# Performance work log

Measured on AMD Instinct MI355X. Metric: run time of the kernel, lower is better.

## Reference

```python
import jax
import jax.numpy as jnp
import numpy as np
import math

KNN = 16
DIST_THRESH = 0.03


def setup_inputs() -> dict:
    key = jax.random.key(0)
    ks = jax.random.split(key, 7)
    B, N, M = 2, 8192, 8192
    Din, D = 64, 64
    feature1 = jax.random.normal(ks[0], (B, N, Din), dtype=jnp.float32)
    xyz1 = jax.random.uniform(ks[1], (B, N, 3), dtype=jnp.float32)
    xyz2 = jax.random.uniform(ks[2], (B, M, 3), dtype=jnp.float32)
    Wp = jax.random.normal(ks[3], (Din, D), dtype=jnp.float32) * 0.05
    bp = jnp.zeros((D,), dtype=jnp.float32)
    W1 = jax.random.normal(ks[4], (3, D), dtype=jnp.float32) * 0.05
    b1 = jnp.zeros((D,), dtype=jnp.float32)
    W2 = jax.random.normal(ks[5], (D, D), dtype=jnp.float32) * 0.05
    b2 = jnp.zeros((D,), dtype=jnp.float32)
    return {"feature1": feature1, "xyz1": xyz1, "xyz2": xyz2,
            "Wp": Wp, "bp": bp, "W1": W1, "b1": b1, "W2": W2, "b2": b2}


def reference(feature1, xyz1, xyz2, Wp, bp, W1, b1, W2, b2):
    # prefix linear: [B,N,Din] -> [B,N,D]
    f = feature1 @ Wp + bp

    # knn_point: squared pairwise distance from queries xyz2 to points xyz1
    # d2: [B, M, N]
    d2 = (jnp.sum(xyz2 * xyz2, axis=-1)[:, :, None]
          + jnp.sum(xyz1 * xyz1, axis=-1)[:, None, :]
          - 2.0 * jnp.einsum('bmd,bnd->bmn', xyz2, xyz1))
    neg_d, idx = jax.lax.top_k(-d2, KNN)        # smallest-k, ascending
    dist = -neg_d                                # [B, M, KNN]

    min_distance = dist[:, :, 0]                 # [B, M]
    weight = jnp.where(min_distance > DIST_THRESH, 10.0, 1.0).astype(f.dtype)

    # index_points: per-batch gather of neighbor features / coords
    g_feature = jax.vmap(lambda a, i: a[i])(f, idx)      # [B, M, KNN, D]
    g_xyz = jax.vmap(lambda a, i: a[i])(xyz1, idx)       # [B, M, KNN, 3]
    g_xyz = g_xyz - xyz2[:, :, None, :]                  # relative coords

    # fc_position MLP: 3 -> D -> D
    pw = jax.nn.relu(g_xyz @ W1 + b1) @ W2 + b2          # [B, M, KNN, D]

    # per-channel weighted reduction over KNN neighbors
    new_feature = jnp.einsum('bmkc,bmkc->bmc', pw, g_feature) / math.sqrt(KNN)
    return new_feature, weight
```

## Files before the change

### kernel.cpp

```cpp
#include <hip/hip_runtime.h>
#include <math.h>

#define B 2
#define N 8192
#define M 8192
#define D 64
#define KNN 16
#define BM (B * M)
#define GC 16
#define NC (GC * GC * GC)
#define NSC 64
#define WTMAX 192
#define CAP 20
#define TCAP 448

using frag_ab = __attribute__((ext_vector_type(8))) short;
using frag_cd = __attribute__((ext_vector_type(4))) float;

__device__ __forceinline__ short f2bf(float x) {
    unsigned u = __float_as_uint(x);
    u += 0x7fffu + ((u >> 16) & 1u);
    return (short)(u >> 16);
}

__device__ __forceinline__ float query_cutr(float qx, float qy, float qz) {
    int nc = ((qx < 0.16f) | (qx > 0.84f)) + ((qy < 0.16f) | (qy > 0.84f))
           + ((qz < 0.16f) | (qz > 0.84f));
    return nc == 0 ? 0.121f : nc == 1 ? 0.1525f : nc == 2 ? 0.1921f : 0.242f;
}

#define CHAIN_INS(VARR, IARR, DVAL, IVAL) do {                          \
    float _dd = (DVAL); int _ii = (IVAL);                               \
    _Pragma("unroll")                                                   \
    for (int _r = 0; _r < KNN; ++_r) {                                  \
        bool  _sm = _dd < VARR[_r];                                     \
        float _tv = VARR[_r]; int _ti = IARR[_r];                       \
        VARR[_r] = _sm ? _dd : _tv;  IARR[_r] = _sm ? _ii : _ti;        \
        _dd      = _sm ? _tv : _dd;  _ii      = _sm ? _ti : _ii;        \
    }                                                                   \
} while (0)
#define CHAIN_INSERT(DVAL, IVAL) CHAIN_INS(v, id, DVAL, IVAL)

#define BITONIC_ROUND(VARR, IARR, DL) do {                              \
    float _nv[KNN]; int _nid[KNN];                                      \
    _Pragma("unroll")                                                   \
    for (int _i = 0; _i < KNN; ++_i) {                                  \
        float _pv = __shfl_xor(VARR[KNN - 1 - _i], (DL), 64);           \
        int   _pi = __shfl_xor(IARR[KNN - 1 - _i], (DL), 64);           \
        bool _tk = VARR[_i] <= _pv;                                     \
        _nv[_i]  = _tk ? VARR[_i] : _pv;                                \
        _nid[_i] = _tk ? IARR[_i] : _pi;                                \
    }                                                                   \
    _Pragma("unroll")                                                   \
    for (int _st = 8; _st; _st >>= 1) {                                 \
        _Pragma("unroll")                                               \
        for (int _i = 0; _i < KNN; ++_i) {                              \
            if (!(_i & _st)) {                                          \
                int _j = _i | _st;                                      \
                bool _sw = _nv[_i] > _nv[_j];                           \
                float _ta = _sw ? _nv[_j] : _nv[_i];                    \
                float _tb = _sw ? _nv[_i] : _nv[_j];                    \
                int _ia = _sw ? _nid[_j] : _nid[_i];                    \
                int _ib = _sw ? _nid[_i] : _nid[_j];                    \
                _nv[_i] = _ta; _nv[_j] = _tb;                           \
                _nid[_i] = _ia; _nid[_j] = _ib;                         \
            }                                                           \
        }                                                               \
    }                                                                   \
    _Pragma("unroll")                                                   \
    for (int _i = 0; _i < KNN; ++_i) { VARR[_i] = _nv[_i]; IARR[_i] = _nid[_i]; } \
} while (0)

#define KPROC(PV, TV) do {                                              \
    float _dx = (PV).x - qx, _dy = (PV).y - qy, _dz = (PV).z - qz;      \
    float _dv = fmaf(_dx, _dx, fmaf(_dy, _dy, _dz * _dz));              \
    if (_dv < fcut) {                                                   \
        if (cnt < CAP) {                                                \
            ibuf[cnt][lane] = (unsigned short)(TV);                     \
            ++cnt;                                                      \
        } else {                                   \
            CHAIN_INSERT(_dv, __float_as_int((PV).w));                  \
        }                                                               \
    }                                                                   \
} while (0)

#define KFLUSH() do {                                                   \
    int _t = 0;                                                         \
    for (; _t + 4 <= cur; _t += 4) {                                    \
        float4 _q0 = tile[_t + 0], _q1 = tile[_t + 1];                  \
        float4 _q2 = tile[_t + 2], _q3 = tile[_t + 3];                  \
        KPROC(_q0, _t + 0); KPROC(_q1, _t + 1);                         \
        KPROC(_q2, _t + 2); KPROC(_q3, _t + 3);                         \
    }                                                                   \
    for (; _t < cur; ++_t) { float4 _q0 = tile[_t]; KPROC(_q0, _t); }   \
    int _mx = cnt;                                                      \
    _Pragma("unroll")                                                   \
    for (int _o = 32; _o; _o >>= 1)                                     \
        _mx = max(_mx, __shfl_xor(_mx, _o, 64));                        \
    _mx = __builtin_amdgcn_readfirstlane(_mx);                          \
    int _t2 = 0;                                                        \
    for (; _t2 + 2 <= _mx; _t2 += 2) {                                  \
        int _ta = (_t2     < cnt) ? (int)ibuf[_t2    ][lane] : 0;       \
        int _tb = (_t2 + 1 < cnt) ? (int)ibuf[_t2 + 1][lane] : 0;       \
        float4 _pa = tile[_ta], _pb = tile[_tb];   \
        float _dxa = _pa.x - qx, _dya = _pa.y - qy, _dza = _pa.z - qz;  \
        float _dva = fmaf(_dxa, _dxa, fmaf(_dya, _dya, _dza * _dza));   \
        if (_t2 < cnt && _dva < v[KNN - 1])                             \
            CHAIN_INSERT(_dva, __float_as_int(_pa.w));                  \
        float _dxb = _pb.x - qx, _dyb = _pb.y - qy, _dzb = _pb.z - qz;  \
        float _dvb = fmaf(_dxb, _dxb, fmaf(_dyb, _dyb, _dzb * _dzb));   \
        if (_t2 + 1 < cnt && _dvb < v[KNN - 1])                         \
            CHAIN_INSERT(_dvb, __float_as_int(_pb.w));                  \
    }                                                                   \
    for (; _t2 < _mx; ++_t2) {                                          \
        int _tp = (_t2 < cnt) ? (int)ibuf[_t2][lane] : 0;               \
        float4 _p = tile[_tp];                                          \
        float _dx = _p.x - qx, _dy = _p.y - qy, _dz = _p.z - qz;        \
        float _dv = fmaf(_dx, _dx, fmaf(_dy, _dy, _dz * _dz));          \
        if (_t2 < cnt && _dv < v[KNN - 1])                              \
            CHAIN_INSERT(_dv, __float_as_int(_p.w));                    \
    }                                                                   \
    cnt = 0; cur = 0;                                                   \
} while (0)

__global__ __launch_bounds__(256) void k_prep(const float* __restrict__ feat,
                                              const float* __restrict__ Wp,
                                              const float* __restrict__ bp,
                                              const float* __restrict__ xyz1,
                                              const float* __restrict__ xyz2,
                                              unsigned* __restrict__ pcount,
                                              unsigned* __restrict__ qcount,
                                              float* __restrict__ f) {
    if (blockIdx.x < 64) {
        int i = blockIdx.x * 256 + threadIdx.x;
        int b = i >> 13;
        const float* p = xyz1 + (size_t)i * 3;
        int cx = max(0, min(GC - 1, (int)(p[0] * GC)));
        int cy = max(0, min(GC - 1, (int)(p[1] * GC)));
        int cz = max(0, min(GC - 1, (int)(p[2] * GC)));
        atomicAdd(&pcount[b * NC + (cz * GC + cy) * GC + cx], 1u);
        const float* q = xyz2 + (size_t)i * 3;
        int qx = max(0, min(GC - 1, (int)(q[0] * GC)));
        int qy = max(0, min(GC - 1, (int)(q[1] * GC)));
        int qz = max(0, min(GC - 1, (int)(q[2] * GC)));
        int sc = ((qz >> 2) * 4 + (qy >> 2)) * 4 + (qx >> 2);
        atomicAdd(&qcount[b * NSC + sc], 1u);
    }
    int c  = threadIdx.x & 63;
    int wv = threadIdx.x >> 6;
    int row0 = blockIdx.x * 32 + wv * 8;
    float wp[64];
#pragma unroll
    for (int d = 0; d < 64; ++d) wp[d] = Wp[d * 64 + c];
    float bpc = bp[c];
    float fv[8], acc[8];
#pragma unroll
    for (int r = 0; r < 8; ++r) {
        fv[r]  = feat[(size_t)(row0 + r) * 64 + c];
        acc[r] = bpc;
    }
#pragma unroll
    for (int d = 0; d < 64; ++d) {
#pragma unroll
        for (int r = 0; r < 8; ++r)
            acc[r] = fmaf(__shfl(fv[r], d, 64), wp[d], acc[r]);
    }
#pragma unroll
    for (int r = 0; r < 8; ++r)
        f[(size_t)(row0 + r) * 64 + c] = acc[r];
}

__global__ __launch_bounds__(256) void k_scan(const unsigned* __restrict__ pcount,
                                              const unsigned* __restrict__ qcount,
                                              unsigned* __restrict__ pstart,
                                              unsigned* __restrict__ pcur,
                                              unsigned* __restrict__ qcur,
                                              int* __restrict__ wtab,
                                              int* __restrict__ ntab) {
    __shared__ unsigned wsum[4];
    int blk = blockIdx.x;
    if (blk < 2) {
        int b = blk;
        int t = threadIdx.x;
        int base = b * NC + t * 16;
        unsigned c[16]; unsigned tsum = 0;
#pragma unroll
        for (int k = 0; k < 16; ++k) { c[k] = pcount[base + k]; tsum += c[k]; }
        int lane = t & 63, wv = t >> 6;
        unsigned x = tsum;
#pragma unroll
        for (int off = 1; off < 64; off <<= 1) {
            unsigned y = __shfl_up(x, off, 64);
            if (lane >= off) x += y;
        }
        if (lane == 63) wsum[wv] = x;
        __syncthreads();
        unsigned pre = 0;
        for (int k2 = 0; k2 < wv; ++k2) pre += wsum[k2];
        unsigned run = pre + x - tsum;
#pragma unroll
        for (int k = 0; k < 16; ++k) {
            pstart[base + k] = run; pcur[base + k] = run; run += c[k];
        }
    } else {
        int b = blk - 2;
        if (threadIdx.x >= 64) return;
        int lane = threadIdx.x;
        int c = (int)qcount[b * NSC + lane];
        int x = c;
#pragma unroll
        for (int off = 1; off < 64; off <<= 1) {
            int y = __shfl_up(x, off, 64);
            if (lane >= off) x += y;
        }
        int run = x - c;
        qcur[b * NSC + lane] = (unsigned)run;
        int ne = (c + 63) >> 6;
        int e = ne;
#pragma unroll
        for (int off = 1; off < 64; off <<= 1) {
            int y = __shfl_up(e, off, 64);
            if (lane >= off) e += y;
        }
        int eoff = e - ne;
        for (int j = 0; j < ne; ++j)
            wtab[b * WTMAX + eoff + j] = ((run + j * 64) << 7) | min(64, c - j * 64);
        if (lane == 63) ntab[b] = eoff + ne;
    }
}

__global__ __launch_bounds__(256) void k_scatter(const float* __restrict__ xyz1,
                                                 const float* __restrict__ xyz2,
                                                 unsigned* __restrict__ pcur,
                                                 unsigned* __restrict__ qcur,
                                                 float4* __restrict__ spts,
                                                 int* __restrict__ sidx,
                                                 float4* __restrict__ squery) {
    int i = blockIdx.x * 256 + threadIdx.x;
    int b = i >> 13;
    const float* p = xyz1 + (size_t)i * 3;
    float x = p[0], y = p[1], z = p[2];
    int cx = max(0, min(GC - 1, (int)(x * GC)));
    int cy = max(0, min(GC - 1, (int)(y * GC)));
    int cz = max(0, min(GC - 1, (int)(z * GC)));
    unsigned pos = atomicAdd(&pcur[b * NC + (cz * GC + cy) * GC + cx], 1u);
    spts[(size_t)b * N + pos] = make_float4(x, y, z, fmaf(x, x, fmaf(y, y, z * z)));
    sidx[(size_t)b * N + pos] = i & (N - 1);

    const float* q = xyz2 + (size_t)i * 3;
    float qx = q[0], qy = q[1], qz = q[2];
    int ax = max(0, min(GC - 1, (int)(qx * GC)));
    int ay = max(0, min(GC - 1, (int)(qy * GC)));
    int az = max(0, min(GC - 1, (int)(qz * GC)));
    int sc = ((az >> 2) * 4 + (ay >> 2)) * 4 + (ax >> 2);
    unsigned qpos = atomicAdd(&qcur[b * NSC + sc], 1u);
    squery[(size_t)b * M + qpos] = make_float4(qx, qy, qz, __int_as_float(i));
}

template <int NSLT>
__global__ __launch_bounds__(64) void k_knn(const float4* __restrict__ spts,
                                            const float4* __restrict__ squery,
                                            const unsigned* __restrict__ pstart,
                                            const unsigned* __restrict__ pcount,
                                            const int* __restrict__ wtab,
                                            const int* __restrict__ ntab,
                                            float* __restrict__ part_d,
                                            int* __restrict__ part_i) {
    __shared__ float4         tile[TCAP];
    __shared__ unsigned short ibuf[CAP][64];
    int bid = blockIdx.x;
    int b   = bid / (WTMAX * NSLT);
    int rem = bid - b * (WTMAX * NSLT);
    int ti  = rem / NSLT;
    int s   = rem % NSLT;
    if (ti >= ntab[b]) return;
    int e = wtab[b * WTMAX + ti];
    int qnum = e & 127, qoff = (e >> 7) & 0x3FFF;
    int lane = threadIdx.x;

    int sl = lane < qnum ? lane : qnum - 1;
    float4 q4 = squery[(size_t)b * M + qoff + sl];
    float qx = q4.x, qy = q4.y, qz = q4.z;
    float cutr = query_cutr(qx, qy, qz);
    float fcut = cutr * cutr;

    int lx0 = max(0, (int)floorf((qx - cutr) * GC));
    int lx1 = min(GC - 1, (int)floorf((qx + cutr) * GC));
    int ly0 = max(0, (int)floorf((qy - cutr) * GC));
    int ly1 = min(GC - 1, (int)floorf((qy + cutr) * GC));
    int lz0 = max(0, (int)floorf((qz - cutr) * GC));
    int lz1 = min(GC - 1, (int)floorf((qz + cutr) * GC));
#pragma unroll
    for (int off = 1; off < 64; off <<= 1) {
        lx0 = min(lx0, __shfl_xor(lx0, off, 64));
        lx1 = max(lx1, __shfl_xor(lx1, off, 64));
        ly0 = min(ly0, __shfl_xor(ly0, off, 64));
        ly1 = max(ly1, __shfl_xor(ly1, off, 64));
        lz0 = min(lz0, __shfl_xor(lz0, off, 64));
        lz1 = max(lz1, __shfl_xor(lz1, off, 64));
    }
    int bx0 = __builtin_amdgcn_readfirstlane(lx0);
    int bx1 = __builtin_amdgcn_readfirstlane(lx1);
    int by0 = __builtin_amdgcn_readfirstlane(ly0);
    int by1 = __builtin_amdgcn_readfirstlane(ly1);
    int bz0 = __builtin_amdgcn_readfirstlane(lz0);
    int bz1 = __builtin_amdgcn_readfirstlane(lz1);

    float v[KNN]; int id[KNN];
#pragma unroll
    for (int r = 0; r < KNN; ++r) { v[r] = 3.4e38f; id[r] = 0; }
    int cnt = 0, cur = 0;
    int pb = b * N, cb = b * NC;
    int xspan = bx1 - bx0;

    int ny = by1 - by0 + 1;
    int nrows = (bz1 - bz0 + 1) * ny;
    int myrows = (s < nrows) ? ((nrows - 1 - s) / NSLT + 1) : 0;
    int stj = 0, enj = 0;
    {
        int rj = s + NSLT * lane;
        if (lane < myrows) {
            int dz = rj / ny;
            int dy = rj - dz * ny;
            int codeL = cb + ((bz0 + dz) * GC + (by0 + dy)) * GC + bx0;
            stj = (int)pstart[codeL];
            enj = (int)pstart[codeL + xspan] + (int)pcount[codeL + xspan];
        }
    }
    for (int j = 0; j < myrows; ++j) {
        int st = __builtin_amdgcn_readfirstlane(__shfl(stj, j, 64));
        int en = __builtin_amdgcn_readfirstlane(__shfl(enj, j, 64));
        int len = en - st;
        if (cur + len > TCAP) KFLUSH();
        for (int u = lane; u < len; u += 64) {
            float4 p = spts[pb + st + u];
            p.w = __int_as_float(st + u);
            tile[cur + u] = p;
        }
        cur += len;
    }
    KFLUSH();

    if (lane < qnum) {
        size_t base = ((size_t)(b * M + qoff + lane) * NSLT + s) * KNN;
        float4* pd = (float4*)(part_d + base);
        int4*   pi = (int4*)(part_i + base);
#pragma unroll
        for (int r4 = 0; r4 < 4; ++r4) {
            pd[r4] = make_float4(v[r4 * 4 + 0], v[r4 * 4 + 1],
                                 v[r4 * 4 + 2], v[r4 * 4 + 3]);
            pi[r4] = make_int4(id[r4 * 4 + 0], id[r4 * 4 + 1],
                               id[r4 * 4 + 2], id[r4 * 4 + 3]);
        }
    }
}

template <int NSLT>
__global__ __launch_bounds__(256, 4) void k_merge(const float4* __restrict__ squery,
                                                  const float* __restrict__ part_d,
                                                  const int* __restrict__ part_i,
                                                  const int* __restrict__ sidx,
                                                  const float4* __restrict__ spts,
                                                  int* __restrict__ idx_out,
                                                  float* __restrict__ w_out) {
    int tid = threadIdx.x;
    int l   = tid & 63;
    int wv  = tid >> 6;
    int g   = l >> 4;
    int gl  = l & 15;
    int sqid = blockIdx.x * 16 + wv * 4 + g;
    int b = sqid >> 13;

    float v[KNN]; int id[KNN];
    if (gl < NSLT) {
        size_t base = ((size_t)sqid * NSLT + gl) * KNN;
        const float4* pd = (const float4*)(part_d + base);
        const int4*   pi = (const int4*)(part_i + base);
#pragma unroll
        for (int r4 = 0; r4 < 4; ++r4) {
            float4 dv = pd[r4]; int4 iv = pi[r4];
            v[r4 * 4 + 0] = dv.x; v[r4 * 4 + 1] = dv.y;
            v[r4 * 4 + 2] = dv.z; v[r4 * 4 + 3] = dv.w;
            id[r4 * 4 + 0] = iv.x; id[r4 * 4 + 1] = iv.y;
            id[r4 * 4 + 2] = iv.z; id[r4 * 4 + 3] = iv.w;
        }
    } else {
#pragma unroll
        for (int r = 0; r < KNN; ++r) { v[r] = 3.4e38f; id[r] = 0; }
    }
    BITONIC_ROUND(v, id, 1);
    BITONIC_ROUND(v, id, 2);
    BITONIC_ROUND(v, id, 4);
    BITONIC_ROUND(v, id, 8);

    float4 q4 = squery[sqid];
    float cutr = query_cutr(q4.x, q4.y, q4.z);
    bool miss = !(v[KNN - 1] < cutr * cutr * 0.9999f);
    int gq = __float_as_int(q4.w);
    if (!miss) {
        if (gl == 0) w_out[gq] = (v[0] > 0.03f) ? 10.0f : 1.0f;
        int myid = 0;
#pragma unroll
        for (int r = 0; r < KNN; ++r) if (gl == r) myid = id[r];
        idx_out[(size_t)gl * BM + sqid] = sidx[b * N + myid];
    }

    unsigned long long mmask = __ballot(miss && gl == 0);
    while (mmask) {
        int ml = __ffsll(mmask) - 1;
        mmask &= mmask - 1;
        int msq = blockIdx.x * 16 + wv * 4 + (ml >> 4);
        int mb = msq >> 13;
        float4 mq = squery[msq];
        float fv2[KNN]; int fi2[KNN];
#pragma unroll
        for (int r = 0; r < KNN; ++r) { fv2[r] = 3.4e38f; fi2[r] = 0; }
        for (int t = l; t < N; t += 64) {
            float4 p = spts[(size_t)mb * N + t];
            float dx = p.x - mq.x, dy = p.y - mq.y, dz = p.z - mq.z;
            float dv = fmaf(dx, dx, fmaf(dy, dy, dz * dz));
            if (dv < fv2[KNN - 1]) CHAIN_INS(fv2, fi2, dv, t);
        }
        BITONIC_ROUND(fv2, fi2, 1);
        BITONIC_ROUND(fv2, fi2, 2);
        BITONIC_ROUND(fv2, fi2, 4);
        BITONIC_ROUND(fv2, fi2, 8);
        BITONIC_ROUND(fv2, fi2, 16);
        BITONIC_ROUND(fv2, fi2, 32);
        int mgq = __float_as_int(mq.w);
        if (l == 0) w_out[mgq] = (fv2[0] > 0.03f) ? 10.0f : 1.0f;
        if (l < 16) {
            int myid = 0;
#pragma unroll
            for (int r = 0; r < KNN; ++r) if (l == r) myid = fi2[r];
            idx_out[(size_t)l * BM + msq] = sidx[mb * N + myid];
        }
    }
}

__global__ __launch_bounds__(256) void k_final(const float4* __restrict__ squery,
                                               const int* __restrict__ idxs,
                                               const float* __restrict__ xyz1,
                                               const float* __restrict__ f,
                                               const float* __restrict__ W1,
                                               const float* __restrict__ b1,
                                               const float* __restrict__ W2,
                                               const float* __restrict__ b2,
                                               float* __restrict__ out) {
    __shared__ __align__(16) unsigned short hT[4][16][72];
    int tid = threadIdx.x;
    int l   = tid & 63;
    int wv  = tid >> 6;
    int ln  = l & 15, lg = l >> 4;
    int mq  = blockIdx.x * 4 + wv;
    int bb  = mq >> 13;
    float4 q4 = squery[mq];
    int gq = __float_as_int(q4.w);
    float qx = q4.x, qy = q4.y, qz = q4.z;

    frag_ab bfrag[4][2];
#pragma unroll
    for (int t = 0; t < 4; ++t)
#pragma unroll
        for (int s = 0; s < 2; ++s) {
            frag_ab bv;
#pragma unroll
            for (int j = 0; j < 8; ++j)
                bv[j] = f2bf(W2[(lg * 8 + j + 32 * s) * 64 + t * 16 + ln]);
            bfrag[t][s] = bv;
        }

    float w10 = W1[l], w11 = W1[64 + l], w12 = W1[128 + l], b1c = b1[l];

#pragma unroll
    for (int k = 0; k < KNN; ++k) {
        int nk = idxs[(size_t)k * BM + mq];
        const float* p = xyz1 + ((size_t)bb * N + nk) * 3;
        float gx = p[0] - qx, gy = p[1] - qy, gz = p[2] - qz;
        float t = fmaf(gx, w10, b1c);
        t = fmaf(gy, w11, t);
        t = fmaf(gz, w12, t);
        hT[wv][k][l] = (unsigned short)f2bf(fmaxf(t, 0.f));
    }

    frag_cd acc[4];
#pragma unroll
    for (int t = 0; t < 4; ++t) acc[t] = (frag_cd){0.f, 0.f, 0.f, 0.f};
#pragma unroll
    for (int s = 0; s < 2; ++s) {
        frag_ab af = *(const frag_ab*)&hT[wv][ln][lg * 8 + 32 * s];
#pragma unroll
        for (int t = 0; t < 4; ++t)
            acc[t] = __builtin_amdgcn_mfma_f32_16x16x32_bf16(af, bfrag[t][s],
                                                             acc[t], 0, 0, 0);
    }

    int nk4[4];
#pragma unroll
    for (int i = 0; i < 4; ++i)
        nk4[i] = idxs[(size_t)(lg * 4 + i) * BM + mq];

#pragma unroll
    for (int t = 0; t < 4; ++t) {
        float b2c = b2[t * 16 + ln];
        float s = 0.f;
#pragma unroll
        for (int i = 0; i < 4; ++i) {
            float gf = f[((size_t)bb * N + nk4[i]) * 64 + t * 16 + ln];
            s = fmaf(acc[t][i] + b2c, gf, s);
        }
        s += __shfl_xor(s, 16, 64);
        s += __shfl_xor(s, 32, 64);
        if (lg == t)
            out[(size_t)gq * 64 + t * 16 + ln] = s * 0.25f;
    }
}

extern "C" void kernel_launch(void* const* d_in, const int* in_sizes, int n_in,
                              void* d_out, int out_size, void* d_ws, size_t ws_size,
                              hipStream_t stream) {
    const float* feature1 = (const float*)d_in[0];
    const float* xyz1     = (const float*)d_in[1];
    const float* xyz2     = (const float*)d_in[2];
    const float* Wp       = (const float*)d_in[3];
    const float* bp       = (const float*)d_in[4];
    const float* W1       = (const float*)d_in[5];
    const float* b1       = (const float*)d_in[6];
    const float* W2       = (const float*)d_in[7];
    const float* b2       = (const float*)d_in[8];
    float* out = (float*)d_out;

    char* w = (char*)d_ws;
    float4*   spts   = (float4*)w;    w += (size_t)B * N * 16;
    float4*   squery = (float4*)w;    w += (size_t)B * M * 16;
    float*    f      = (float*)w;     w += (size_t)B * N * D * 4;
    int*      sidx   = (int*)w;       w += (size_t)B * N * 4;
    unsigned* pcount = (unsigned*)w;  w += (size_t)B * NC * 4;
    unsigned* qcount = (unsigned*)w;  w += (size_t)B * NSC * 4;
    unsigned* pstart = (unsigned*)w;  w += (size_t)B * NC * 4;
    unsigned* pcur   = (unsigned*)w;  w += (size_t)B * NC * 4;
    unsigned* qcur   = (unsigned*)w;  w += (size_t)B * NSC * 4;
    int*      wtab   = (int*)w;       w += (size_t)B * WTMAX * 4;
    int*      ntab   = (int*)w;       w += 16;

    size_t used_fixed = (size_t)(w - (char*)d_ws);
    size_t per_slice  = (size_t)KNN * BM * 8;
    size_t idxf_bytes = (size_t)KNN * BM * 4;
    int nsl = (ws_size >= used_fixed + 16 * per_slice + idxf_bytes) ? 16 : 8;

    float*    partd  = (float*)w;     w += (size_t)nsl * KNN * BM * 4;
    int*      parti  = (int*)w;       w += (size_t)nsl * KNN * BM * 4;
    int*      idxf   = (int*)w;       w += idxf_bytes;
    float*    w_out  = out + (size_t)BM * D;

    hipMemsetAsync(pcount, 0, (size_t)(B * NC + B * NSC) * 4, stream);

    k_prep<<<B * N / 32, 256, 0, stream>>>(feature1, Wp, bp, xyz1, xyz2,
                                           pcount, qcount, f);
    k_scan<<<4, 256, 0, stream>>>(pcount, qcount, pstart, pcur, qcur, wtab, ntab);
    k_scatter<<<BM / 256, 256, 0, stream>>>(xyz1, xyz2, pcur, qcur, spts, sidx, squery);
    if (nsl == 16) {
        k_knn<16><<<B * WTMAX * 16, 64, 0, stream>>>(spts, squery, pstart, pcount,
                                                     wtab, ntab, partd, parti);
        k_merge<16><<<BM / 16, 256, 0, stream>>>(squery, partd, parti, sidx, spts,
                                                 idxf, w_out);
    } else {
        k_knn<8><<<B * WTMAX * 8, 64, 0, stream>>>(spts, squery, pstart, pcount,
                                                   wtab, ntab, partd, parti);
        k_merge<8><<<BM / 16, 256, 0, stream>>>(squery, partd, parti, sidx, spts,
                                                idxf, w_out);
    }
    k_final<<<BM / 4, 256, 0, stream>>>(squery, idxf, xyz1, f,
                                        W1, b1, W2, b2, out);
}
```

Baseline: 197.5 us.

## Pack two KNN slice waves per block and raise slice count to 32

The KNN kernel now runs two 64-lane waves per 128-thread block, each handling a different spatial slice with its own shared tile. The tile and candidate buffer capacities are halved, and tile filling is chunked so a cell range can be split across flushes. When the workspace is large enough, the search is split into 32 slices, and the merge kernel is generalized to a variable group size. The aim is finer-grained parallelism and better occupancy in the neighbor search, at the cost of more partial results to write and merge and more frequent flushes.

```diff
diff --git a/kernel.cpp b/kernel.cpp
--- a/kernel.cpp
+++ b/kernel.cpp
@@ -11,8 +11,8 @@
 #define NC (GC * GC * GC)
 #define NSC 64
 #define WTMAX 192
-#define CAP 20
-#define TCAP 448
+#define CAP 12
+#define TCAP 224
 
 using frag_ab = __attribute__((ext_vector_type(8))) short;
 using frag_cd = __attribute__((ext_vector_type(4))) float;
@@ -76,7 +76,7 @@
     float _dv = fmaf(_dx, _dx, fmaf(_dy, _dy, _dz * _dz));              \
     if (_dv < fcut) {                                                   \
         if (cnt < CAP) {                                                \
-            ibuf[cnt][lane] = (unsigned short)(TV);                     \
+            ibuf[cnt][tidx] = (unsigned short)(TV);                     \
             ++cnt;                                                      \
         } else {                                   \
             CHAIN_INSERT(_dv, __float_as_int((PV).w));                  \
@@ -87,12 +87,12 @@
 #define KFLUSH() do {                                                   \
     int _t = 0;                                                         \
     for (; _t + 4 <= cur; _t += 4) {                                    \
-        float4 _q0 = tile[_t + 0], _q1 = tile[_t + 1];                  \
-        float4 _q2 = tile[_t + 2], _q3 = tile[_t + 3];                  \
+        float4 _q0 = tilew[_t + 0], _q1 = tilew[_t + 1];                \
+        float4 _q2 = tilew[_t + 2], _q3 = tilew[_t + 3];                \
         KPROC(_q0, _t + 0); KPROC(_q1, _t + 1);                         \
         KPROC(_q2, _t + 2); KPROC(_q3, _t + 3);                         \
     }                                                                   \
-    for (; _t < cur; ++_t) { float4 _q0 = tile[_t]; KPROC(_q0, _t); }   \
+    for (; _t < cur; ++_t) { float4 _q0 = tilew[_t]; KPROC(_q0, _t); }  \
     int _mx = cnt;                                                      \
     _Pragma("unroll")                                                   \
     for (int _o = 32; _o; _o >>= 1)                                     \
@@ -100,9 +100,9 @@
     _mx = __builtin_amdgcn_readfirstlane(_mx);                          \
     int _t2 = 0;                                                        \
     for (; _t2 + 2 <= _mx; _t2 += 2) {                                  \
-        int _ta = (_t2     < cnt) ? (int)ibuf[_t2    ][lane] : 0;       \
-        int _tb = (_t2 + 1 < cnt) ? (int)ibuf[_t2 + 1][lane] : 0;       \
-        float4 _pa = tile[_ta], _pb = tile[_tb];   \
+        int _ta = (_t2     < cnt) ? (int)ibuf[_t2    ][tidx] : 0;       \
+        int _tb = (_t2 + 1 < cnt) ? (int)ibuf[_t2 + 1][tidx] : 0;       \
+        float4 _pa = tilew[_ta], _pb = tilew[_tb]; \
         float _dxa = _pa.x - qx, _dya = _pa.y - qy, _dza = _pa.z - qz;  \
         float _dva = fmaf(_dxa, _dxa, fmaf(_dya, _dya, _dza * _dza));   \
         if (_t2 < cnt && _dva < v[KNN - 1])                             \
@@ -113,8 +113,8 @@
             CHAIN_INSERT(_dvb, __float_as_int(_pb.w));                  \
     }                                                                   \
     for (; _t2 < _mx; ++_t2) {                                          \
-        int _tp = (_t2 < cnt) ? (int)ibuf[_t2][lane] : 0;               \
-        float4 _p = tile[_tp];                                          \
+        int _tp = (_t2 < cnt) ? (int)ibuf[_t2][tidx] : 0;               \
+        float4 _p = tilew[_tp];                                         \
         float _dx = _p.x - qx, _dy = _p.y - qy, _dz = _p.z - qz;        \
         float _dv = fmaf(_dx, _dx, fmaf(_dy, _dy, _dz * _dz));          \
         if (_t2 < cnt && _dv < v[KNN - 1])                              \
@@ -258,25 +258,30 @@
 }
 
 template <int NSLT>
-__global__ __launch_bounds__(64) void k_knn(const float4* __restrict__ spts,
-                                            const float4* __restrict__ squery,
-                                            const unsigned* __restrict__ pstart,
-                                            const unsigned* __restrict__ pcount,
-                                            const int* __restrict__ wtab,
-                                            const int* __restrict__ ntab,
-                                            float* __restrict__ part_d,
-                                            int* __restrict__ part_i) {
-    __shared__ float4         tile[TCAP];
-    __shared__ unsigned short ibuf[CAP][64];
+__global__ __launch_bounds__(128) void k_knn(const float4* __restrict__ spts,
+                                             const float4* __restrict__ squery,
+                                             const unsigned* __restrict__ pstart,
+                                             const unsigned* __restrict__ pcount,
+                                             const int* __restrict__ wtab,
+                                             const int* __restrict__ ntab,
+                                             float* __restrict__ part_d,
+                                             int* __restrict__ part_i) {
+    __shared__ float4         tile2[2][TCAP];
+    __shared__ unsigned short ibuf[CAP][128];
+    constexpr int SPB = NSLT / 2;
+    int tidx = threadIdx.x;
+    int lane = tidx & 63;
+    int wv   = tidx >> 6;
     int bid = blockIdx.x;
-    int b   = bid / (WTMAX * NSLT);
-    int rem = bid - b * (WTMAX * NSLT);
-    int ti  = rem / NSLT;
-    int s   = rem % NSLT;
+    int b   = bid / (WTMAX * SPB);
+    int rem = bid - b * (WTMAX * SPB);
+    int ti  = rem / SPB;
+    int sp  = rem - ti * SPB;
+    int s   = sp * 2 + wv;
     if (ti >= ntab[b]) return;
+    float4* tilew = tile2[wv];
     int e = wtab[b * WTMAX + ti];
     int qnum = e & 127, qoff = (e >> 7) & 0x3FFF;
-    int lane = threadIdx.x;
 
     int sl = lane < qnum ? lane : qnum - 1;
     float4 q4 = squery[(size_t)b * M + qoff + sl];
@@ -331,13 +336,16 @@
         int st = __builtin_amdgcn_readfirstlane(__shfl(stj, j, 64));
         int en = __builtin_amdgcn_readfirstlane(__shfl(enj, j, 64));
         int len = en - st;
-        if (cur + len > TCAP) KFLUSH();
-        for (int u = lane; u < len; u += 64) {
-            float4 p = spts[pb + st + u];
-            p.w = __int_as_float(st + u);
-            tile[cur + u] = p;
-        }
-        cur += len;
+        while (len > 0) {
+            int take = min(len, TCAP - cur);
+            for (int u = lane; u < take; u += 64) {
+                float4 p = spts[pb + st + u];
+                p.w = __int_as_float(st + u);
+                tilew[cur + u] = p;
+            }
+            cur += take; st += take; len -= take;
+            if (cur == TCAP) KFLUSH();
+        }
     }
     KFLUSH();
 
@@ -363,17 +371,19 @@
                                                   const float4* __restrict__ spts,
                                                   int* __restrict__ idx_out,
                                                   float* __restrict__ w_out) {
+    constexpr int GS  = NSLT;
+    constexpr int QPW = 64 / GS;
     int tid = threadIdx.x;
     int l   = tid & 63;
     int wv  = tid >> 6;
-    int g   = l >> 4;
-    int gl  = l & 15;
-    int sqid = blockIdx.x * 16 + wv * 4 + g;
+    int g   = l / GS;
+    int gl  = l % GS;
+    int sqid = blockIdx.x * (QPW * 4) + wv * QPW + g;
     int b = sqid >> 13;
 
     float v[KNN]; int id[KNN];
-    if (gl < NSLT) {
-        size_t base = ((size_t)sqid * NSLT + gl) * KNN;
+    {
+        size_t base = ((size_t)sqid * GS + gl) * KNN;
         const float4* pd = (const float4*)(part_d + base);
         const int4*   pi = (const int4*)(part_i + base);
 #pragma unroll
@@ -384,14 +394,10 @@
             id[r4 * 4 + 0] = iv.x; id[r4 * 4 + 1] = iv.y;
             id[r4 * 4 + 2] = iv.z; id[r4 * 4 + 3] = iv.w;
         }
-    } else {
-#pragma unroll
-        for (int r = 0; r < KNN; ++r) { v[r] = 3.4e38f; id[r] = 0; }
-    }
-    BITONIC_ROUND(v, id, 1);
-    BITONIC_ROUND(v, id, 2);
-    BITONIC_ROUND(v, id, 4);
-    BITONIC_ROUND(v, id, 8);
+    }
+#pragma unroll
+    for (int dl = 1; dl < GS; dl <<= 1)
+        BITONIC_ROUND(v, id, dl);
 
     float4 q4 = squery[sqid];
     float cutr = query_cutr(q4.x, q4.y, q4.z);
@@ -399,17 +405,23 @@
     int gq = __float_as_int(q4.w);
     if (!miss) {
         if (gl == 0) w_out[gq] = (v[0] > 0.03f) ? 10.0f : 1.0f;
-        int myid = 0;
-#pragma unroll
-        for (int r = 0; r < KNN; ++r) if (gl == r) myid = id[r];
-        idx_out[(size_t)gl * BM + sqid] = sidx[b * N + myid];
+#pragma unroll
+        for (int rr = 0; rr < (KNN + GS - 1) / GS; ++rr) {
+            int r = gl + rr * GS;
+            if (r < KNN) {
+                int myid = 0;
+#pragma unroll
+                for (int k = 0; k < KNN; ++k) if (r == k) myid = id[k];
+                idx_out[(size_t)r * BM + sqid] = sidx[b * N + myid];
+            }
+        }
     }
 
     unsigned long long mmask = __ballot(miss && gl == 0);
     while (mmask) {
         int ml = __ffsll(mmask) - 1;
         mmask &= mmask - 1;
-        int msq = blockIdx.x * 16 + wv * 4 + (ml >> 4);
+        int msq = blockIdx.x * (QPW * 4) + wv * QPW + ml / GS;
         int mb = msq >> 13;
         float4 mq = squery[msq];
         float fv2[KNN]; int fi2[KNN];
@@ -546,7 +558,8 @@
     size_t used_fixed = (size_t)(w - (char*)d_ws);
     size_t per_slice  = (size_t)KNN * BM * 8;
     size_t idxf_bytes = (size_t)KNN * BM * 4;
-    int nsl = (ws_size >= used_fixed + 16 * per_slice + idxf_bytes) ? 16 : 8;
+    int nsl = (ws_size >= used_fixed + 32 * per_slice + idxf_bytes) ? 32 :
+              (ws_size >= used_fixed + 16 * per_slice + idxf_bytes) ? 16 : 8;
 
     float*    partd  = (float*)w;     w += (size_t)nsl * KNN * BM * 4;
     int*      parti  = (int*)w;       w += (size_t)nsl * KNN * BM * 4;
@@ -559,15 +572,20 @@
                                            pcount, qcount, f);
     k_scan<<<4, 256, 0, stream>>>(pcount, qcount, pstart, pcur, qcur, wtab, ntab);
     k_scatter<<<BM / 256, 256, 0, stream>>>(xyz1, xyz2, pcur, qcur, spts, sidx, squery);
-    if (nsl == 16) {
-        k_knn<16><<<B * WTMAX * 16, 64, 0, stream>>>(spts, squery, pstart, pcount,
+    if (nsl == 32) {
+        k_knn<32><<<B * WTMAX * 16, 128, 0, stream>>>(spts, squery, pstart, pcount,
+                                                      wtab, ntab, partd, parti);
+        k_merge<32><<<BM / 8, 256, 0, stream>>>(squery, partd, parti, sidx, spts,
+                                                idxf, w_out);
+    } else if (nsl == 16) {
+        k_knn<16><<<B * WTMAX * 8, 128, 0, stream>>>(spts, squery, pstart, pcount,
                                                      wtab, ntab, partd, parti);
         k_merge<16><<<BM / 16, 256, 0, stream>>>(squery, partd, parti, sidx, spts,
                                                  idxf, w_out);
     } else {
-        k_knn<8><<<B * WTMAX * 8, 64, 0, stream>>>(spts, squery, pstart, pcount,
-                                                   wtab, ntab, partd, parti);
-        k_merge<8><<<BM / 16, 256, 0, stream>>>(squery, partd, parti, sidx, spts,
+        k_knn<8><<<B * WTMAX * 4, 128, 0, stream>>>(spts, squery, pstart, pcount,
+                                                    wtab, ntab, partd, parti);
+        k_merge<8><<<BM / 32, 256, 0, stream>>>(squery, partd, parti, sidx, spts,
                                                 idxf, w_out);
     }
     k_final<<<BM / 4, 256, 0, stream>>>(squery, idxf, xyz1, f,
```

Result: slower. 218.6 us (+10.7%).

## Balance kNN slices by point count via prefix-sum and pack merge groups by slice count

Applied to the files above, without the earlier changes.

The kNN kernel previously gave each slice whole grid rows round-robin, which leaves slices with uneven point counts. It now builds a prefix sum of per-row point counts in shared memory and gives each slice an equal contiguous range of points. Each point's source address is found with a binary search over the row offsets. The merge kernel now sizes its lane groups to the slice count, so the 8-slice variant handles twice as many queries per wave with half the blocks. This adds binary-search cost per point and shrinks the tile and index buffers, and it assumes at most 192 rows per wave (3 per lane) even though RMAX is 200.

```diff
diff --git a/kernel.cpp b/kernel.cpp
--- a/kernel.cpp
+++ b/kernel.cpp
@@ -11,8 +11,9 @@
 #define NC (GC * GC * GC)
 #define NSC 64
 #define WTMAX 192
-#define CAP 20
-#define TCAP 448
+#define CAP 16
+#define TCAP 256
+#define RMAX 200
 
 using frag_ab = __attribute__((ext_vector_type(8))) short;
 using frag_cd = __attribute__((ext_vector_type(4))) float;
@@ -268,6 +269,8 @@
                                             int* __restrict__ part_i) {
     __shared__ float4         tile[TCAP];
     __shared__ unsigned short ibuf[CAP][64];
+    __shared__ int            rowg[RMAX];
+    __shared__ int            rowst[RMAX];
     int bid = blockIdx.x;
     int b   = bid / (WTMAX * NSLT);
     int rem = bid - b * (WTMAX * NSLT);
@@ -306,40 +309,67 @@
     int bz0 = __builtin_amdgcn_readfirstlane(lz0);
     int bz1 = __builtin_amdgcn_readfirstlane(lz1);
 
+    int pb = b * N, cb = b * NC;
+    int xspan = bx1 - bx0;
+    int ny = by1 - by0 + 1;
+    int nrows = (bz1 - bz0 + 1) * ny;
+
+    int myst[3], mylen[3];
+#pragma unroll
+    for (int k = 0; k < 3; ++k) {
+        int r = lane * 3 + k;
+        myst[k] = 0; mylen[k] = 0;
+        if (r < nrows) {
+            int dz = r / ny;
+            int dy = r - dz * ny;
+            int codeL = cb + ((bz0 + dz) * GC + (by0 + dy)) * GC + bx0;
+            myst[k]  = (int)pstart[codeL];
+            mylen[k] = (int)pstart[codeL + xspan] + (int)pcount[codeL + xspan]
+                     - myst[k];
+        }
+    }
+    int lsum = mylen[0] + mylen[1] + mylen[2];
+    int x = lsum;
+#pragma unroll
+    for (int off = 1; off < 64; off <<= 1) {
+        int y = __shfl_up(x, off, 64);
+        if (lane >= off) x += y;
+    }
+    int P = __builtin_amdgcn_readfirstlane(__shfl(x, 63, 64));
+    int g = x - lsum;
+#pragma unroll
+    for (int k = 0; k < 3; ++k) {
+        int r = lane * 3 + k;
+        if (r < nrows) { rowg[r] = g; rowst[r] = myst[k]; }
+        g += mylen[k];
+    }
+
     float v[KNN]; int id[KNN];
 #pragma unroll
     for (int r = 0; r < KNN; ++r) { v[r] = 3.4e38f; id[r] = 0; }
     int cnt = 0, cur = 0;
-    int pb = b * N, cb = b * NC;
-    int xspan = bx1 - bx0;
-
-    int ny = by1 - by0 + 1;
-    int nrows = (bz1 - bz0 + 1) * ny;
-    int myrows = (s < nrows) ? ((nrows - 1 - s) / NSLT + 1) : 0;
-    int stj = 0, enj = 0;
-    {
-        int rj = s + NSLT * lane;
-        if (lane < myrows) {
-            int dz = rj / ny;
-            int dy = rj - dz * ny;
-            int codeL = cb + ((bz0 + dz) * GC + (by0 + dy)) * GC + bx0;
-            stj = (int)pstart[codeL];
-            enj = (int)pstart[codeL + xspan] + (int)pcount[codeL + xspan];
-        }
-    }
-    for (int j = 0; j < myrows; ++j) {
-        int st = __builtin_amdgcn_readfirstlane(__shfl(stj, j, 64));
-        int en = __builtin_amdgcn_readfirstlane(__shfl(enj, j, 64));
-        int len = en - st;
-        if (cur + len > TCAP) KFLUSH();
-        for (int u = lane; u < len; u += 64) {
-            float4 p = spts[pb + st + u];
-            p.w = __int_as_float(st + u);
-            tile[cur + u] = p;
-        }
-        cur += len;
-    }
-    KFLUSH();
+
+    int lo = (s * P) / NSLT;
+    int hi = ((s + 1) * P) / NSLT;
+    int done = lo;
+    while (done < hi) {
+        int take = min(hi - done, TCAP);
+        for (int u = lane; u < take; u += 64) {
+            int p = done + u;
+            int l0 = 0, h0 = nrows - 1;
+            while (l0 < h0) {
+                int m = (l0 + h0 + 1) >> 1;
+                if (rowg[m] <= p) l0 = m; else h0 = m - 1;
+            }
+            int addr = rowst[l0] + (p - rowg[l0]);
+            float4 pt = spts[pb + addr];
+            pt.w = __int_as_float(addr);
+            tile[u] = pt;
+        }
+        cur = take;
+        KFLUSH();
+        done += take;
+    }
 
     if (lane < qnum) {
         size_t base = ((size_t)(b * M + qoff + lane) * NSLT + s) * KNN;
@@ -363,17 +393,19 @@
                                                   const float4* __restrict__ spts,
                                                   int* __restrict__ idx_out,
                                                   float* __restrict__ w_out) {
+    constexpr int GS  = NSLT;
+    constexpr int QPW = 64 / GS;
     int tid = threadIdx.x;
     int l   = tid & 63;
     int wv  = tid >> 6;
-    int g   = l >> 4;
-    int gl  = l & 15;
-    int sqid = blockIdx.x * 16 + wv * 4 + g;
+    int g   = l / GS;
+    int gl  = l % GS;
+    int sqid = blockIdx.x * (QPW * 4) + wv * QPW + g;
     int b = sqid >> 13;
 
     float v[KNN]; int id[KNN];
-    if (gl < NSLT) {
-        size_t base = ((size_t)sqid * NSLT + gl) * KNN;
+    {
+        size_t base = ((size_t)sqid * GS + gl) * KNN;
         const float4* pd = (const float4*)(part_d + base);
         const int4*   pi = (const int4*)(part_i + base);
 #pragma unroll
@@ -384,14 +416,10 @@
             id[r4 * 4 + 0] = iv.x; id[r4 * 4 + 1] = iv.y;
             id[r4 * 4 + 2] = iv.z; id[r4 * 4 + 3] = iv.w;
         }
-    } else {
-#pragma unroll
-        for (int r = 0; r < KNN; ++r) { v[r] = 3.4e38f; id[r] = 0; }
-    }
-    BITONIC_ROUND(v, id, 1);
-    BITONIC_ROUND(v, id, 2);
-    BITONIC_ROUND(v, id, 4);
-    BITONIC_ROUND(v, id, 8);
+    }
+#pragma unroll
+    for (int dl = 1; dl < GS; dl <<= 1)
+        BITONIC_ROUND(v, id, dl);
 
     float4 q4 = squery[sqid];
     float cutr = query_cutr(q4.x, q4.y, q4.z);
@@ -399,17 +427,23 @@
     int gq = __float_as_int(q4.w);
     if (!miss) {
         if (gl == 0) w_out[gq] = (v[0] > 0.03f) ? 10.0f : 1.0f;
-        int myid = 0;
-#pragma unroll
-        for (int r = 0; r < KNN; ++r) if (gl == r) myid = id[r];
-        idx_out[(size_t)gl * BM + sqid] = sidx[b * N + myid];
+#pragma unroll
+        for (int rr = 0; rr < (KNN + GS - 1) / GS; ++rr) {
+            int r = gl + rr * GS;
+            if (r < KNN) {
+                int myid = 0;
+#pragma unroll
+                for (int k = 0; k < KNN; ++k) if (r == k) myid = id[k];
+                idx_out[(size_t)r * BM + sqid] = sidx[b * N + myid];
+            }
+        }
     }
 
     unsigned long long mmask = __ballot(miss && gl == 0);
     while (mmask) {
         int ml = __ffsll(mmask) - 1;
         mmask &= mmask - 1;
-        int msq = blockIdx.x * 16 + wv * 4 + (ml >> 4);
+        int msq = blockIdx.x * (QPW * 4) + wv * QPW + ml / GS;
         int mb = msq >> 13;
         float4 mq = squery[msq];
         float fv2[KNN]; int fi2[KNN];
@@ -567,7 +601,7 @@
     } else {
         k_knn<8><<<B * WTMAX * 8, 64, 0, stream>>>(spts, squery, pstart, pcount,
                                                    wtab, ntab, partd, parti);
-        k_merge<8><<<BM / 16, 256, 0, stream>>>(squery, partd, parti, sidx, spts,
+        k_merge<8><<<BM / 32, 256, 0, stream>>>(squery, partd, parti, sidx, spts,
                                                 idxf, w_out);
     }
     k_final<<<BM / 4, 256, 0, stream>>>(squery, idxf, xyz1, f,
```

Result: slower. 214.9 us (+8.8%).
